# Kernel optimization log

Hardware: AMD Instinct MI355X
Metric: run time of the kernel (lower is better)

## Reference

```python
import math
import jax, jax.numpy as jnp
import numpy as np

B, T, HIDDEN = 2, 2048, 1024
H, HKV, D = 16, 16, 64


def _rope_tables(T, D):
    inv_freq = 1.0 / (10000.0 ** (jnp.arange(0, D, 2, dtype=jnp.float32) / D))
    t = jnp.arange(T, dtype=jnp.float32)
    freqs = jnp.outer(t, inv_freq)               # [T, D/2]
    emb = jnp.concatenate([freqs, freqs], axis=-1)  # [T, D]
    return jnp.cos(emb), jnp.sin(emb)


def setup_inputs() -> dict:
    key = jax.random.key(0)
    k1, k2, k3 = jax.random.split(key, 3)
    hidden_states = jax.random.normal(k1, (B, T, HIDDEN), dtype=jnp.float32)
    cos, sin = _rope_tables(T, D)
    # trunc-normal-ish init, std = 1/sqrt(fan_in)
    w_qkv = jax.random.normal(k2, ((H + 2 * HKV) * D, HIDDEN), dtype=jnp.float32) / math.sqrt(HIDDEN)
    w_o = jax.random.normal(k3, (HIDDEN, H * D), dtype=jnp.float32) / math.sqrt(H * D)
    return {"hidden_states": hidden_states, "cos": cos, "sin": sin, "w_qkv": w_qkv, "w_o": w_o}


def _rotate_half(x):
    x1, x2 = jnp.split(x, 2, axis=-1)
    return jnp.concatenate([-x2, x1], axis=-1)


def reference(hidden_states, cos, sin, w_qkv, w_o):
    b, t, _ = hidden_states.shape
    # fused QKV projection: [B,T,(H+2*HKV)*D]
    qkv = jnp.einsum('bti,oi->bto', hidden_states, w_qkv)
    qkv = qkv.reshape(b, t, H + 2 * HKV, D)
    q = qkv[:, :, :H]                    # [B,T,H,D]
    k = qkv[:, :, H:H + HKV]             # [B,T,HKV,D]
    v = qkv[:, :, H + HKV:]              # [B,T,HKV,D]
    # inline RoPE; cos/sin broadcast over heads
    c = cos[:, None, :]
    s = sin[:, None, :]
    q = q * c + _rotate_half(q) * s
    k = k * c + _rotate_half(k) * s
    scale = 1.0 / math.sqrt(D)
    attn_scores = jnp.einsum('bthd,bThd->bhtT', q, k) * scale  # [B,H,T,T]
    mask = jnp.tril(jnp.ones((t, t), dtype=bool))
    attn_scores = jnp.where(mask[None, None, :, :], attn_scores, -1e9)
    attn = jax.nn.softmax(attn_scores, axis=-1)
    context = jnp.einsum('bhtT,bThd->bthd', attn, v).reshape(b, t, H * D)
    return jnp.einsum('bti,oi->bto', context, w_o)
```

## Files before the change

### kernel.cpp

```cpp
#include <hip/hip_runtime.h>

typedef __bf16 bf16_t;
typedef __bf16 bf16x4 __attribute__((ext_vector_type(4)));
typedef __bf16 bf16x8 __attribute__((ext_vector_type(8)));
typedef float f32x4 __attribute__((ext_vector_type(4)));
typedef unsigned int u32x2 __attribute__((ext_vector_type(2)));
typedef unsigned long long u64;

#define MFMA16(a, b, c) __builtin_amdgcn_mfma_f32_16x16x32_bf16((a), (b), (c), 0, 0, 0)

#define LDG2LDS16(g, l)                                                        \
    __builtin_amdgcn_global_load_lds(                                          \
        (const __attribute__((address_space(1))) void*)(g),                    \
        (__attribute__((address_space(3))) void*)(l), 16, 0, 0)

#if __has_builtin(__builtin_amdgcn_exp2f)
#define EXP2(x) __builtin_amdgcn_exp2f(x)
#else
#define EXP2(x) exp2f(x)
#endif

__device__ inline bf16x8 load8(const float* p) {
    const f32x4 a = *(const f32x4*)p;
    const f32x4 b = *(const f32x4*)(p + 4);
    bf16x8 r;
#pragma unroll
    for (int i = 0; i < 4; i++) { r[i] = (bf16_t)a[i]; r[4 + i] = (bf16_t)b[i]; }
    return r;
}

__device__ inline u32x2 as2(bf16x4 v) {
    u32x2 r;
    __builtin_memcpy(&r, &v, 8);
    return r;
}

__device__ inline bf16x4 shfl4(bf16x4 v, int src) {
    u64 x;
    __builtin_memcpy(&x, &v, 8);
    x = __shfl(x, src, 64);
    bf16x4 r;
    __builtin_memcpy(&r, &x, 8);
    return r;
}

__global__ __launch_bounds__(256) void convert_kernel(const float* __restrict__ hs,
                                                      const float* __restrict__ wqkv,
                                                      const float* __restrict__ wo,
                                                      bf16_t* __restrict__ outb) {
    const size_t c = ((size_t)blockIdx.x * 256 + threadIdx.x) * 8;
    const float* src;
    size_t off;
    if (c < 4194304) { src = hs; off = c; }
    else if (c < 7340032) { src = wqkv; off = c - 4194304; }
    else { src = wo; off = c - 7340032; }
    *(bf16x8*)(outb + c) = load8(src + off);
}


template <int MODE, int NDIM, int BM>
__global__ __launch_bounds__(256) void gemm_bt(const bf16_t* __restrict__ A,
                                               const bf16_t* __restrict__ B,
                                               float* __restrict__ outp,
                                               bf16_t* __restrict__ q_ws,
                                               bf16_t* __restrict__ k_ws,
                                               bf16_t* __restrict__ v_ws,
                                               const float* __restrict__ cosb,
                                               const float* __restrict__ sinb) {
    constexpr int K = 1024;
    constexpr int IM = BM / 32;
    __shared__ __align__(16) bf16_t As[BM * 32];
    __shared__ __align__(16) bf16_t Bs[128 * 32];

    const int tid = threadIdx.x;
    const int w = tid >> 6;
    const int lane = tid & 63;
    const int lr = lane & 15;
    const int quad = lane >> 4;
    const int m0 = blockIdx.y * BM;
    const int n0 = blockIdx.x * 128;
    const int wm = (w & 1) * (BM / 2);
    const int wn = (w >> 1) * 64;

    const int srow = tid >> 2;
    const int skk = (((tid & 3) ^ ((tid >> 3) & 3)) * 8);
    const bf16_t* gA0 = A + (size_t)(m0 + srow) * K + skk;
    const bf16_t* gA1 = gA0 + (size_t)64 * K;
    const bf16_t* gB0 = B + (size_t)(n0 + srow) * K + skk;
    const bf16_t* gB1 = gB0 + (size_t)64 * K;
    bf16_t* lA0 = As + w * 512;
    bf16_t* lA1 = As + 2048 + w * 512;
    bf16_t* lB0 = Bs + w * 512;
    bf16_t* lB1 = Bs + 2048 + w * 512;

    const int qsw = (quad ^ ((lr >> 1) & 3)) * 8;

    f32x4 acc[IM][4] = {};

    for (int k0 = 0; k0 < K; k0 += 32) {
        LDG2LDS16(gA0 + k0, lA0);
        if constexpr (BM == 128) LDG2LDS16(gA1 + k0, lA1);
        LDG2LDS16(gB0 + k0, lB0);
        LDG2LDS16(gB1 + k0, lB1);
        __syncthreads();

        bf16x8 af[IM], bfm[4];
#pragma unroll
        for (int im = 0; im < IM; im++)
            af[im] = *(const bf16x8*)&As[(wm + im * 16 + lr) * 32 + qsw];
#pragma unroll
        for (int in = 0; in < 4; in++)
            bfm[in] = *(const bf16x8*)&Bs[(wn + in * 16 + lr) * 32 + qsw];
#pragma unroll
        for (int im = 0; im < IM; im++)
#pragma unroll
            for (int in = 0; in < 4; in++)
                acc[im][in] = MFMA16(af[im], bfm[in], acc[im][in]);
        __syncthreads();
    }

    if constexpr (MODE == 0) {
#pragma unroll
        for (int im = 0; im < IM; im++)
#pragma unroll
            for (int in = 0; in < 4; in++)
#pragma unroll
                for (int r = 0; r < 4; r++) {
                    const int m = m0 + wm + im * 16 + quad * 4 + r;
                    const int n = n0 + wn + in * 16 + lr;
                    outp[(size_t)m * NDIM + n] = acc[im][in][r];
                }
    } else {
        const int j = (n0 + wn) >> 6;
        if (j < 32) {
            const bool isq = (j < 16);
            const float qs = 0.125f * 1.44269504089f;
#pragma unroll
            for (int im = 0; im < IM; im++) {
#pragma unroll
                for (int r = 0; r < 4; r++) {
                    const int m = m0 + wm + im * 16 + quad * 4 + r;
                    const int b = m >> 11;
                    const int t = m & 2047;
#pragma unroll
                    for (int in = 0; in < 2; in++) {
                        const int d = in * 16 + lr;
                        const float x1 = acc[im][in][r];
                        const float x2 = acc[im][in + 2][r];
                        const float c = cosb[t * 64 + d];
                        const float s = sinb[t * 64 + d];
                        float y1 = x1 * c - x2 * s;
                        float y2 = x2 * c + x1 * s;
                        if (isq) {
                            y1 *= qs; y2 *= qs;
                            const size_t base =
                                ((size_t)(b * 16 + j) * 2048 + t) * 64 + d;
                            q_ws[base] = (bf16_t)y1;
                            q_ws[base + 32] = (bf16_t)y2;
                        } else {
                            const int bh = b * 16 + (j - 16);
                            const size_t off =
                                ((size_t)(bh * 128 + (t >> 4)) * 2) * 512 +
                                ((t & 15) + (d >> 3) * 16) * 8 + (d & 7);
                            k_ws[off] = (bf16_t)y1;
                            k_ws[off + 512] = (bf16_t)y2;
                        }
                    }
                }
            }
        } else {
#pragma unroll
            for (int im = 0; im < IM; im++)
#pragma unroll
                for (int in = 0; in < 4; in++)
#pragma unroll
                    for (int r = 0; r < 4; r++) {
                        const int m = m0 + wm + im * 16 + quad * 4 + r;
                        const int b = m >> 11;
                        const int t = m & 2047;
                        const int d = in * 16 + lr;
                        const int bh = b * 16 + (j - 32);
                        const size_t off =
                            ((size_t)(bh * 64 + (t >> 5)) * 4 + (d >> 4)) * 512 +
                            ((d & 15) + ((t & 31) >> 3) * 16) * 8 + (t & 7);
                        v_ws[off] = (bf16_t)acc[im][in][r];
                    }
        }
    }
}

__device__ inline void flash_tile(int qt, int quad, int lr, int query,
                                  const bf16_t* __restrict__ kbase,
                                  const bf16_t* __restrict__ vbase,
                                  bf16x8 qlo, bf16x8 qhi,
                                  f32x4* o, float& lrun) {
    bf16x8 kc[8];
#pragma unroll
    for (int n = 0; n < 4; n++) {
        kc[2 * n] = *(const bf16x8*)(kbase + (size_t)(n * 2) * 512);
        kc[2 * n + 1] = *(const bf16x8*)(kbase + (size_t)(n * 2 + 1) * 512);
    }

    for (int kb = 0; kb <= qt; kb++) {
        bf16x8 vv[2][4];
#pragma unroll
        for (int hh = 0; hh < 2; hh++)
#pragma unroll
            for (int n = 0; n < 4; n++)
                vv[hh][n] = *(const bf16x8*)(vbase +
                    (size_t)((kb * 2 + hh) * 4 + n) * 512);

        const int kbn = (kb < qt) ? kb + 1 : kb;
        bf16x8 kn[8];
#pragma unroll
        for (int n = 0; n < 4; n++) {
            kn[2 * n] = *(const bf16x8*)(kbase + (size_t)((kbn * 4 + n) * 2) * 512);
            kn[2 * n + 1] = *(const bf16x8*)(kbase + (size_t)((kbn * 4 + n) * 2 + 1) * 512);
        }

        const int u0 = kb * 64;
        f32x4 s[4];
#pragma unroll
        for (int n = 0; n < 4; n++) {
            const f32x4 z = {};
            s[n] = MFMA16(kc[2 * n], qlo, z);
            s[n] = MFMA16(kc[2 * n + 1], qhi, s[n]);
        }

        if (kb == qt) {
#pragma unroll
            for (int n = 0; n < 4; n++)
#pragma unroll
                for (int r = 0; r < 4; r++)
                    if (u0 + n * 16 + quad * 4 + r > query) s[n][r] = -1e9f;
        }

        f32x4 p[4];
#pragma unroll
        for (int n = 0; n < 4; n++)
#pragma unroll
            for (int r = 0; r < 4; r++) p[n][r] = EXP2(s[n][r]);

        lrun += ((p[0][0] + p[0][1]) + (p[0][2] + p[0][3])) +
                ((p[1][0] + p[1][1]) + (p[1][2] + p[1][3])) +
                ((p[2][0] + p[2][1]) + (p[2][2] + p[2][3])) +
                ((p[3][0] + p[3][1]) + (p[3][2] + p[3][3]));

        bf16x4 pb[4];
#pragma unroll
        for (int n = 0; n < 4; n++)
#pragma unroll
            for (int r = 0; r < 4; r++) pb[n][r] = (bf16_t)p[n][r];

#pragma unroll
        for (int hh = 0; hh < 2; hh++) {
            bf16x8 pf;
#if __has_builtin(__builtin_amdgcn_permlane16_swap) && \
    __has_builtin(__builtin_amdgcn_permlane32_swap)
            const u32x2 P0 = as2(pb[2 * hh]);
            const u32x2 P1 = as2(pb[2 * hh + 1]);
            const u32x2 s1a = __builtin_amdgcn_permlane16_swap(P0[0], P0[1], false, false);
            const u32x2 s1b = __builtin_amdgcn_permlane16_swap(P1[0], P1[1], false, false);
            const u32x2 s2a = __builtin_amdgcn_permlane32_swap(s1a[0], s1b[0], false, false);
            const u32x2 s2b = __builtin_amdgcn_permlane32_swap(s1a[1], s1b[1], false, false);
            const u32x2 s3a = __builtin_amdgcn_permlane16_swap(s2a[0], s2a[1], false, false);
            const u32x2 s3b = __builtin_amdgcn_permlane16_swap(s2b[0], s2b[1], false, false);
            const unsigned pfd[4] = {s3a[0], s3a[1], s3b[0], s3b[1]};
            __builtin_memcpy(&pf, pfd, 16);
#else
            const int srcLow = ((quad & 1) << 5) + lr;
            const int srcHigh = srcLow + 16;
            const bool loSel = (quad < 2);
            const bf16x4 a0 = shfl4(pb[2 * hh], srcLow);
            const bf16x4 a1 = shfl4(pb[2 * hh + 1], srcLow);
            const bf16x4 b0 = shfl4(pb[2 * hh], srcHigh);
            const bf16x4 b1 = shfl4(pb[2 * hh + 1], srcHigh);
            const bf16x4 lo = loSel ? a0 : a1;
            const bf16x4 hi = loSel ? b0 : b1;
#pragma unroll
            for (int r = 0; r < 4; r++) { pf[r] = lo[r]; pf[4 + r] = hi[r]; }
#endif
#pragma unroll
            for (int n = 0; n < 4; n++)
                o[n] = MFMA16(vv[hh][n], pf, o[n]);
        }

#pragma unroll
        for (int i = 0; i < 8; i++) kc[i] = kn[i];
    }
}

__global__ __launch_bounds__(256) void attn_kernel(const bf16_t* __restrict__ q_ws,
                                                   const bf16_t* __restrict__ k_ws,
                                                   const bf16_t* __restrict__ v_ws,
                                                   bf16_t* __restrict__ ctx) {
    const int tid = threadIdx.x;
    const int w = tid >> 6;
    const int lane = tid & 63;
    const int lr = lane & 15;
    const int quad = lane >> 4;
    const int bh = blockIdx.x & 31;
    const int pr = blockIdx.x >> 5;
    const int b = bh >> 4;
    const int hd = bh & 15;

    const bf16_t* kbase = k_ws + (size_t)bh * 131072 + lane * 8;
    const bf16_t* vbase = v_ws + (size_t)bh * 131072 + lane * 8;

#pragma unroll
    for (int half = 0; half < 2; half++) {
        const int qt = half ? (31 - pr) : pr;
        const int trow = qt * 64 + w * 16;
        const int query = trow + lr;

        const bf16_t* qb = q_ws + ((size_t)bh * 2048 + trow + lr) * 64 + quad * 8;
        const bf16x8 qlo = *(const bf16x8*)qb;
        const bf16x8 qhi = *(const bf16x8*)(qb + 32);

        f32x4 o[4] = {};
        float lrun = 0.0f;
        flash_tile(qt, quad, lr, query, kbase, vbase, qlo, qhi, o, lrun);

        lrun += __shfl_xor(lrun, 16);
        lrun += __shfl_xor(lrun, 32);

        const float inv = 1.0f / fmaxf(lrun, 1e-30f);
        const size_t base = ((size_t)b * 2048 + query) * 1024 + hd * 64 + quad * 4;
#pragma unroll
        for (int n = 0; n < 4; n++) {
            bf16x4 ob;
#pragma unroll
            for (int r = 0; r < 4; r++) ob[r] = (bf16_t)(o[n][r] * inv);
            *(bf16x4*)&ctx[base + n * 16] = ob;
        }
    }
}

extern "C" void kernel_launch(void* const* d_in, const int* in_sizes, int n_in,
                              void* d_out, int out_size, void* d_ws, size_t ws_size,
                              hipStream_t stream) {
    const float* hs = (const float*)d_in[0];
    const float* cosb = (const float*)d_in[1];
    const float* sinb = (const float*)d_in[2];
    const float* wqkv = (const float*)d_in[3];
    const float* wo = (const float*)d_in[4];
    float* out = (float*)d_out;

    char* ws = (char*)d_ws;
    bf16_t* hs_b = (bf16_t*)(ws);
    bf16_t* wqkv_b = hs_b + 4194304;
    bf16_t* wo_b = hs_b + 7340032;
    bf16_t* q_ws = (bf16_t*)(ws + (size_t)(16u << 20));
    bf16_t* k_ws = (bf16_t*)(ws + (size_t)(24u << 20));
    bf16_t* v_ws = (bf16_t*)(ws + (size_t)(32u << 20));
    bf16_t* ctx = (bf16_t*)(ws);

    const dim3 blk(256);

    convert_kernel<<<dim3(4096), blk, 0, stream>>>(hs, wqkv, wo, hs_b);

    gemm_bt<1, 3072, 128><<<dim3(24, 32), blk, 0, stream>>>(
        hs_b, wqkv_b, nullptr, q_ws, k_ws, v_ws, cosb, sinb);

    attn_kernel<<<dim3(512), blk, 0, stream>>>(q_ws, k_ws, v_ws, ctx);

    gemm_bt<0, 1024, 64><<<dim3(8, 64), blk, 0, stream>>>(
        ctx, wo_b, out, nullptr, nullptr, nullptr, nullptr, nullptr);
}
```

Measured before the change: 178.0 us.

## Stage K/V tiles through double-buffered LDS with async global-to-LDS loads

Replaces per-wave direct global loads of K and V fragments with a cooperative double-buffered shared-memory pipeline. Each of the four waves issues global_load_lds copies for the next key block while computing on the current one. This shares each K/V tile across the waves instead of every wave fetching it separately, and overlaps loads with compute. It adds a block-wide barrier and a full wait every iteration, which could serialise waves and limit the overlap.

```diff
diff --git a/kernel.cpp b/kernel.cpp
--- a/kernel.cpp
+++ b/kernel.cpp
@@ -189,111 +189,13 @@
     }
 }
 
-__device__ inline void flash_tile(int qt, int quad, int lr, int query,
-                                  const bf16_t* __restrict__ kbase,
-                                  const bf16_t* __restrict__ vbase,
-                                  bf16x8 qlo, bf16x8 qhi,
-                                  f32x4* o, float& lrun) {
-    bf16x8 kc[8];
-#pragma unroll
-    for (int n = 0; n < 4; n++) {
-        kc[2 * n] = *(const bf16x8*)(kbase + (size_t)(n * 2) * 512);
-        kc[2 * n + 1] = *(const bf16x8*)(kbase + (size_t)(n * 2 + 1) * 512);
-    }
-
-    for (int kb = 0; kb <= qt; kb++) {
-        bf16x8 vv[2][4];
-#pragma unroll
-        for (int hh = 0; hh < 2; hh++)
-#pragma unroll
-            for (int n = 0; n < 4; n++)
-                vv[hh][n] = *(const bf16x8*)(vbase +
-                    (size_t)((kb * 2 + hh) * 4 + n) * 512);
-
-        const int kbn = (kb < qt) ? kb + 1 : kb;
-        bf16x8 kn[8];
-#pragma unroll
-        for (int n = 0; n < 4; n++) {
-            kn[2 * n] = *(const bf16x8*)(kbase + (size_t)((kbn * 4 + n) * 2) * 512);
-            kn[2 * n + 1] = *(const bf16x8*)(kbase + (size_t)((kbn * 4 + n) * 2 + 1) * 512);
-        }
-
-        const int u0 = kb * 64;
-        f32x4 s[4];
-#pragma unroll
-        for (int n = 0; n < 4; n++) {
-            const f32x4 z = {};
-            s[n] = MFMA16(kc[2 * n], qlo, z);
-            s[n] = MFMA16(kc[2 * n + 1], qhi, s[n]);
-        }
-
-        if (kb == qt) {
-#pragma unroll
-            for (int n = 0; n < 4; n++)
-#pragma unroll
-                for (int r = 0; r < 4; r++)
-                    if (u0 + n * 16 + quad * 4 + r > query) s[n][r] = -1e9f;
-        }
-
-        f32x4 p[4];
-#pragma unroll
-        for (int n = 0; n < 4; n++)
-#pragma unroll
-            for (int r = 0; r < 4; r++) p[n][r] = EXP2(s[n][r]);
-
-        lrun += ((p[0][0] + p[0][1]) + (p[0][2] + p[0][3])) +
-                ((p[1][0] + p[1][1]) + (p[1][2] + p[1][3])) +
-                ((p[2][0] + p[2][1]) + (p[2][2] + p[2][3])) +
-                ((p[3][0] + p[3][1]) + (p[3][2] + p[3][3]));
-
-        bf16x4 pb[4];
-#pragma unroll
-        for (int n = 0; n < 4; n++)
-#pragma unroll
-            for (int r = 0; r < 4; r++) pb[n][r] = (bf16_t)p[n][r];
-
-#pragma unroll
-        for (int hh = 0; hh < 2; hh++) {
-            bf16x8 pf;
-#if __has_builtin(__builtin_amdgcn_permlane16_swap) && \
-    __has_builtin(__builtin_amdgcn_permlane32_swap)
-            const u32x2 P0 = as2(pb[2 * hh]);
-            const u32x2 P1 = as2(pb[2 * hh + 1]);
-            const u32x2 s1a = __builtin_amdgcn_permlane16_swap(P0[0], P0[1], false, false);
-            const u32x2 s1b = __builtin_amdgcn_permlane16_swap(P1[0], P1[1], false, false);
-            const u32x2 s2a = __builtin_amdgcn_permlane32_swap(s1a[0], s1b[0], false, false);
-            const u32x2 s2b = __builtin_amdgcn_permlane32_swap(s1a[1], s1b[1], false, false);
-            const u32x2 s3a = __builtin_amdgcn_permlane16_swap(s2a[0], s2a[1], false, false);
-            const u32x2 s3b = __builtin_amdgcn_permlane16_swap(s2b[0], s2b[1], false, false);
-            const unsigned pfd[4] = {s3a[0], s3a[1], s3b[0], s3b[1]};
-            __builtin_memcpy(&pf, pfd, 16);
-#else
-            const int srcLow = ((quad & 1) << 5) + lr;
-            const int srcHigh = srcLow + 16;
-            const bool loSel = (quad < 2);
-            const bf16x4 a0 = shfl4(pb[2 * hh], srcLow);
-            const bf16x4 a1 = shfl4(pb[2 * hh + 1], srcLow);
-            const bf16x4 b0 = shfl4(pb[2 * hh], srcHigh);
-            const bf16x4 b1 = shfl4(pb[2 * hh + 1], srcHigh);
-            const bf16x4 lo = loSel ? a0 : a1;
-            const bf16x4 hi = loSel ? b0 : b1;
-#pragma unroll
-            for (int r = 0; r < 4; r++) { pf[r] = lo[r]; pf[4 + r] = hi[r]; }
-#endif
-#pragma unroll
-            for (int n = 0; n < 4; n++)
-                o[n] = MFMA16(vv[hh][n], pf, o[n]);
-        }
-
-#pragma unroll
-        for (int i = 0; i < 8; i++) kc[i] = kn[i];
-    }
-}
-
 __global__ __launch_bounds__(256) void attn_kernel(const bf16_t* __restrict__ q_ws,
                                                    const bf16_t* __restrict__ k_ws,
                                                    const bf16_t* __restrict__ v_ws,
                                                    bf16_t* __restrict__ ctx) {
+    __shared__ __align__(16) bf16_t Ks[2][4096];
+    __shared__ __align__(16) bf16_t Vs[2][4096];
+
     const int tid = threadIdx.x;
     const int w = tid >> 6;
     const int lane = tid & 63;
@@ -304,8 +206,20 @@
     const int b = bh >> 4;
     const int hd = bh & 15;
 
-    const bf16_t* kbase = k_ws + (size_t)bh * 131072 + lane * 8;
-    const bf16_t* vbase = v_ws + (size_t)bh * 131072 + lane * 8;
+    const bf16_t* kws = k_ws + (size_t)bh * 131072;
+    const bf16_t* vws = v_ws + (size_t)bh * 131072;
+    const int soff = w * 512 + lane * 8;
+    const int lo8 = lane * 8;
+
+#define ASTAGE(kb, buf)                                                        \
+    {                                                                          \
+        LDG2LDS16(kws + (size_t)(kb) * 4096 + soff, &Ks[buf][w * 512]);        \
+        LDG2LDS16(kws + (size_t)(kb) * 4096 + 2048 + soff,                     \
+                  &Ks[buf][2048 + w * 512]);                                   \
+        LDG2LDS16(vws + (size_t)(kb) * 4096 + soff, &Vs[buf][w * 512]);        \
+        LDG2LDS16(vws + (size_t)(kb) * 4096 + 2048 + soff,                     \
+                  &Vs[buf][2048 + w * 512]);                                   \
+    }
 
 #pragma unroll
     for (int half = 0; half < 2; half++) {
@@ -319,7 +233,92 @@
 
         f32x4 o[4] = {};
         float lrun = 0.0f;
-        flash_tile(qt, quad, lr, query, kbase, vbase, qlo, qhi, o, lrun);
+
+        ASTAGE(0, 0);
+        asm volatile("s_waitcnt vmcnt(0)" ::: "memory");
+        __builtin_amdgcn_s_barrier();
+        asm volatile("" ::: "memory");
+
+        for (int kb = 0; kb <= qt; kb++) {
+            const int buf = kb & 1;
+            if (kb < qt) ASTAGE(kb + 1, buf ^ 1);
+
+            f32x4 s[4];
+#pragma unroll
+            for (int n = 0; n < 4; n++) {
+                const bf16x8 k0 = *(const bf16x8*)&Ks[buf][(2 * n) * 512 + lo8];
+                const bf16x8 k1 = *(const bf16x8*)&Ks[buf][(2 * n + 1) * 512 + lo8];
+                const f32x4 z = {};
+                s[n] = MFMA16(k0, qlo, z);
+                s[n] = MFMA16(k1, qhi, s[n]);
+            }
+
+            const int u0 = kb * 64;
+            if (kb == qt) {
+#pragma unroll
+                for (int n = 0; n < 4; n++)
+#pragma unroll
+                    for (int r = 0; r < 4; r++)
+                        if (u0 + n * 16 + quad * 4 + r > query) s[n][r] = -1e9f;
+            }
+
+            f32x4 p[4];
+#pragma unroll
+            for (int n = 0; n < 4; n++)
+#pragma unroll
+                for (int r = 0; r < 4; r++) p[n][r] = EXP2(s[n][r]);
+
+            lrun += ((p[0][0] + p[0][1]) + (p[0][2] + p[0][3])) +
+                    ((p[1][0] + p[1][1]) + (p[1][2] + p[1][3])) +
+                    ((p[2][0] + p[2][1]) + (p[2][2] + p[2][3])) +
+                    ((p[3][0] + p[3][1]) + (p[3][2] + p[3][3]));
+
+            bf16x4 pb[4];
+#pragma unroll
+            for (int n = 0; n < 4; n++)
+#pragma unroll
+                for (int r = 0; r < 4; r++) pb[n][r] = (bf16_t)p[n][r];
+
+#pragma unroll
+            for (int hh = 0; hh < 2; hh++) {
+                bf16x8 pf;
+#if __has_builtin(__builtin_amdgcn_permlane16_swap) && \
+    __has_builtin(__builtin_amdgcn_permlane32_swap)
+                const u32x2 P0 = as2(pb[2 * hh]);
+                const u32x2 P1 = as2(pb[2 * hh + 1]);
+                const u32x2 s1a = __builtin_amdgcn_permlane16_swap(P0[0], P0[1], false, false);
+                const u32x2 s1b = __builtin_amdgcn_permlane16_swap(P1[0], P1[1], false, false);
+                const u32x2 s2a = __builtin_amdgcn_permlane32_swap(s1a[0], s1b[0], false, false);
+                const u32x2 s2b = __builtin_amdgcn_permlane32_swap(s1a[1], s1b[1], false, false);
+                const u32x2 s3a = __builtin_amdgcn_permlane16_swap(s2a[0], s2a[1], false, false);
+                const u32x2 s3b = __builtin_amdgcn_permlane16_swap(s2b[0], s2b[1], false, false);
+                const unsigned pfd[4] = {s3a[0], s3a[1], s3b[0], s3b[1]};
+                __builtin_memcpy(&pf, pfd, 16);
+#else
+                const int srcLow = ((quad & 1) << 5) + lr;
+                const int srcHigh = srcLow + 16;
+                const bool loSel = (quad < 2);
+                const bf16x4 a0 = shfl4(pb[2 * hh], srcLow);
+                const bf16x4 a1 = shfl4(pb[2 * hh + 1], srcLow);
+                const bf16x4 b0 = shfl4(pb[2 * hh], srcHigh);
+                const bf16x4 b1 = shfl4(pb[2 * hh + 1], srcHigh);
+                const bf16x4 lo = loSel ? a0 : a1;
+                const bf16x4 hi = loSel ? b0 : b1;
+#pragma unroll
+                for (int r = 0; r < 4; r++) { pf[r] = lo[r]; pf[4 + r] = hi[r]; }
+#endif
+#pragma unroll
+                for (int n = 0; n < 4; n++) {
+                    const bf16x8 vvf =
+                        *(const bf16x8*)&Vs[buf][(hh * 4 + n) * 512 + lo8];
+                    o[n] = MFMA16(vvf, pf, o[n]);
+                }
+            }
+
+            asm volatile("s_waitcnt lgkmcnt(0) vmcnt(0)" ::: "memory");
+            __builtin_amdgcn_s_barrier();
+            asm volatile("" ::: "memory");
+        }
 
         lrun += __shfl_xor(lrun, 16);
         lrun += __shfl_xor(lrun, 32);
@@ -334,6 +333,7 @@
             *(bf16x4*)&ctx[base + n * 16] = ob;
         }
     }
+#undef ASTAGE
 }
 
 extern "C" void kernel_launch(void* const* d_in, const int* in_sizes, int n_in,
```

New measurement: 172.9 us. 1.03x faster.
